# Kernel optimization log

Measured on AMD Instinct MI355X. Metric: run time of the kernel, lower is better.

Reference implementation:

```python
import jax, jax.numpy as jnp
import numpy as np

B, N, C, CODE, DIRB = 4, 321408, 3, 7, 2
K_PRE, K_POST = 1000, 300
IOU_THR, SCORE_THR, DIR_OFFSET = 0.5, 0.05, 0.0
POST_RANGE = np.array([0.0, -39.68, -5.0, 69.12, 39.68, 5.0], dtype=np.float32)


def setup_inputs() -> dict:
    key = jax.random.key(0)
    k1, k2, k3, k4 = jax.random.split(key, 4)
    box_preds = jax.random.normal(k1, (B, N, CODE), jnp.float32) * 0.3
    # shift logits down so sigmoid scores straddle the 0.05 threshold realistically
    cls_preds = jax.random.normal(k2, (B, N, C), jnp.float32) * 2.0 - 2.0
    dir_preds = jax.random.normal(k3, (B, N, DIRB), jnp.float32)
    ka, kb, kc = jax.random.split(k4, 3)
    xy = jax.random.uniform(ka, (N, 2), jnp.float32) * jnp.array([69.12, 79.36], jnp.float32) + jnp.array([0.0, -39.68], jnp.float32)
    z = jnp.full((N, 1), -1.0, jnp.float32)
    dims = jax.random.uniform(kb, (N, 3), jnp.float32, minval=1.0, maxval=4.0)
    rot = jax.random.randint(kc, (N, 1), 0, 2).astype(jnp.float32) * np.float32(np.pi / 2)
    anchors = jnp.concatenate([xy, z, dims, rot], axis=-1)
    return {"box_preds": box_preds, "cls_preds": cls_preds, "dir_preds": dir_preds, "anchors": anchors}


def _decode(deltas, anchors):
    # SECOND / PointPillars GroundBox3dCoder decode. anchors: [x,y,z,w,l,h,r]
    xa, ya, za, wa, la, ha, ra = (anchors[..., i] for i in range(7))
    xt, yt, zt, wt, lt, ht, rt = (deltas[..., i] for i in range(7))
    za = za + ha * 0.5
    diag = jnp.sqrt(la * la + wa * wa)
    xg = xt * diag + xa
    yg = yt * diag + ya
    zg = zt * ha + za
    wg = jnp.exp(wt) * wa
    lg = jnp.exp(lt) * la
    hg = jnp.exp(ht) * ha
    zg = zg - hg * 0.5
    rg = rt + ra
    return jnp.stack([xg, yg, zg, wg, lg, hg, rg], axis=-1)


def _nms_single(boxes7, scores, valid):
    # boxes_for_nms = box[:, [0,1,3,4,-1]] -> rotated (x,y,w,l,r); standup AABB of corners
    x, y, w, l, r = boxes7[:, 0], boxes7[:, 1], boxes7[:, 3], boxes7[:, 4], boxes7[:, 6]
    c, s = jnp.abs(jnp.cos(r)), jnp.abs(jnp.sin(r))
    hx = 0.5 * (w * c + l * s)   # half-extent of rotated corners along x
    hy = 0.5 * (w * s + l * c)
    x1, x2, y1, y2 = x - hx, x + hx, y - hy, y + hy
    area = (x2 - x1) * (y2 - y1)
    ix = jnp.clip(jnp.minimum(x2[:, None], x2[None, :]) - jnp.maximum(x1[:, None], x1[None, :]), 0.0)
    iy = jnp.clip(jnp.minimum(y2[:, None], y2[None, :]) - jnp.maximum(y1[:, None], y1[None, :]), 0.0)
    inter = ix * iy
    union = area[:, None] + area[None, :] - inter
    iou = jnp.where(union > 0, inter / jnp.maximum(union, 1e-12), 0.0)
    iou = jax.lax.stop_gradient(iou)
    idxs = jnp.arange(K_PRE)

    def body(keep, i):
        sup = keep[i] & (iou[i] > IOU_THR) & (idxs > i)
        return keep & ~sup, None

    keep, _ = jax.lax.scan(body, valid, idxs)
    rank = jnp.cumsum(keep) - 1                       # rank among kept (score order)
    pos = jnp.argsort(jnp.where(keep, rank, K_PRE))   # stable: kept-in-order first
    sel = pos[:K_POST]
    return sel, keep[sel]


def reference(box_preds, cls_preds, dir_preds, anchors):
    decoded = _decode(box_preds, anchors[None, :, :])          # [B,N,7]
    probs = jax.nn.sigmoid(cls_preds)                          # [B,N,C]
    top_scores = probs.max(axis=-1)
    top_labels = probs.argmax(axis=-1).astype(jnp.int32)
    dir_labels = dir_preds.argmax(axis=-1).astype(jnp.int32)
    valid = top_scores >= SCORE_THR
    sc_masked = jnp.where(valid, top_scores, -1.0)
    sc_k, idx = jax.lax.top_k(sc_masked, K_PRE)                # [B,K_PRE]
    boxes_k = jnp.take_along_axis(decoded, idx[..., None], axis=1)
    labels_k = jnp.take_along_axis(top_labels, idx, axis=1)
    dir_k = jnp.take_along_axis(dir_labels, idx, axis=1)
    valid_k = sc_k >= SCORE_THR
    sel, keep = jax.vmap(_nms_single)(boxes_k, sc_k, valid_k)  # [B,K_POST]
    boxes = jnp.take_along_axis(boxes_k, sel[..., None], axis=1)
    scores = jnp.take_along_axis(sc_k, sel, axis=1)
    labels = jnp.take_along_axis(labels_k, sel, axis=1)
    dirs = jnp.take_along_axis(dir_k, sel, axis=1)
    # direction flip: add pi where predicted direction disagrees with yaw sign
    opp = ((boxes[..., 6] - DIR_OFFSET) > 0) ^ (dirs == 1)
    r_fixed = boxes[..., 6] + jnp.where(opp, np.float32(np.pi), np.float32(0.0))
    boxes = jnp.concatenate([boxes[..., :6], r_fixed[..., None]], axis=-1)
    # post center-range filter
    lo = jnp.asarray(POST_RANGE[:3])
    hi = jnp.asarray(POST_RANGE[3:])
    in_range = jnp.all(boxes[..., :3] >= lo, axis=-1) & jnp.all(boxes[..., :3] <= hi, axis=-1)
    valid_out = keep & in_range
    boxes = jnp.where(valid_out[..., None], boxes, 0.0)
    scores = jnp.where(valid_out, scores, 0.0)
    labels = jnp.where(valid_out, labels, 0)
    return boxes, labels, scores, valid_out
```

## Files before the change

kernel.cpp:

```cpp
#include <hip/hip_runtime.h>
#include <stdint.h>

typedef unsigned long long u64;
typedef unsigned int u32;

#define BB 4
#define NN 321408
#define K_PRE 1000
#define K_POST 300
#define CAP 4096
#define NW 16
#define SCORE_THR 0.05f
#define IOU_THR 0.5f
#define SB 314
#define CH2 1024
#define NBINS 576
#define BIN0 0xBD4Cu
#define RED 8
#define RCH 40

__device__ __forceinline__ float sigm(float x) { return 1.0f / (1.0f + expf(-x)); }

__device__ __forceinline__ u32 mkkey(float mx) {
    float s = sigm(mx);
    return (s >= SCORE_THR) ? (__float_as_uint(s) | 0x80000000u) : 0u;
}

__global__ void k_score_hist(const float* __restrict__ cls, u32* __restrict__ key, u32* __restrict__ bh) {
    __shared__ u32 h1[NBINS], h2[NBINS];
    int bb = blockIdx.x, tid = threadIdx.x;
    int b = bb / SB, c = bb % SB;
    for (int i = tid; i < NBINS; i += 256) h1[i] = 0;
    __syncthreads();
    int a0 = c * CH2 + tid * 4;
    if (a0 < NN) {
        const float4* c4 = (const float4*)(cls + ((size_t)b * NN + a0) * 3);
        float4 v0 = c4[0], v1 = c4[1], v2 = c4[2];
        uint4 o;
        o.x = mkkey(fmaxf(v0.x, fmaxf(v0.y, v0.z)));
        o.y = mkkey(fmaxf(v0.w, fmaxf(v1.x, v1.y)));
        o.z = mkkey(fmaxf(v1.z, fmaxf(v1.w, v2.x)));
        o.w = mkkey(fmaxf(v2.y, fmaxf(v2.z, v2.w)));
        *((uint4*)(key + (size_t)b * NN + a0)) = o;
        if (o.x) atomicAdd(&h1[min((o.x >> 16) - BIN0, (u32)(NBINS - 1))], 1u);
        if (o.y) atomicAdd(&h1[min((o.y >> 16) - BIN0, (u32)(NBINS - 1))], 1u);
        if (o.z) atomicAdd(&h1[min((o.z >> 16) - BIN0, (u32)(NBINS - 1))], 1u);
        if (o.w) atomicAdd(&h1[min((o.w >> 16) - BIN0, (u32)(NBINS - 1))], 1u);
    }
    __syncthreads();
    u32* src = h1; u32* dst = h2;
    for (int off = 1; off < NBINS; off <<= 1) {
        for (int i = tid; i < NBINS; i += 256)
            dst[i] = src[i] + ((i + off < NBINS) ? src[i + off] : 0u);
        __syncthreads();
        u32* t = src; src = dst; dst = t;
    }
    for (int i = tid; i < NBINS; i += 256) bh[(size_t)bb * NBINS + i] = src[i];
}

__global__ __launch_bounds__(64) void k_red(const u32* __restrict__ bh, u32* __restrict__ part) {
    int blk = blockIdx.x, tid = threadIdx.x;
    int b = blk / (RED * 9);
    int r = (blk / 9) % RED;
    int g = blk % 9;
    int f = g * 64 + tid;
    int s0 = r * RCH, s1 = s0 + RCH; if (s1 > SB) s1 = SB;
    const u32* base = bh + (size_t)(b * SB + s0) * NBINS + f;
    u32 acc = 0;
    int n = s1 - s0;
    #pragma unroll 8
    for (int s = 0; s < n; ++s) acc += base[(size_t)s * NBINS];
    part[(size_t)(b * RED + r) * NBINS + f] = acc;
}

__global__ __launch_bounds__(256) void k_scatterT(const u32* __restrict__ key, const u32* __restrict__ part,
                                                  const u32* __restrict__ bh, u32* __restrict__ cnt,
                                                  u64* __restrict__ cand) {
    __shared__ u32 tot[NBINS];
    __shared__ u32 wtot[4];
    __shared__ u32 sTf;
    int bb = blockIdx.x, tid = threadIdx.x;
    int b = bb / SB, c = bb % SB;
    int lane = tid & 63, wv = tid >> 6;
    for (int f = tid; f < NBINS; f += 256) {
        u32 x = 0;
        #pragma unroll
        for (int r = 0; r < RED; ++r) x += part[(size_t)(b * RED + r) * NBINS + f];
        tot[f] = x;
    }
    __syncthreads();
    u32 tv = tot[0];
    u32 target = (tv < K_PRE) ? tv : K_PRE;
    if (target == 0) {
        if (c == 0 && tid == 0) cnt[b] = 0;
        return;
    }
    for (int f = tid; f < NBINS; f += 256) {
        u32 cge = tot[f];
        u32 cnx = (f + 1 < NBINS) ? tot[f + 1] : 0u;
        if (cge >= target && cnx < target) sTf = (u32)f;
    }
    __syncthreads();
    u32 Tf = sTf;
    if (c == 0 && tid == 0) cnt[b] = tot[Tf];
    u32 m = 0;
    if (tid < c) m = bh[(size_t)(b * SB + tid) * NBINS + Tf];
    if (tid + 256 < c) m += bh[(size_t)(b * SB + tid + 256) * NBINS + Tf];
    #pragma unroll
    for (int o = 32; o > 0; o >>= 1) m += __shfl_down(m, o);
    if (lane == 0) wtot[wv] = m;
    __syncthreads();
    u32 boffc = wtot[0] + wtot[1] + wtot[2] + wtot[3];
    __syncthreads();
    u32 T16 = BIN0 + Tf;
    int a0 = c * CH2 + tid * 4;
    uint4 kk = make_uint4(0u, 0u, 0u, 0u);
    if (a0 < NN) kk = *((const uint4*)(key + (size_t)b * NN + a0));
    u32 ks[4] = {kk.x, kk.y, kk.z, kk.w};
    u32 f4[4];
    #pragma unroll
    for (int e = 0; e < 4; ++e) f4[e] = (u32)((ks[e] != 0) && ((ks[e] >> 16) >= T16));
    u32 tc = f4[0] + f4[1] + f4[2] + f4[3];
    u32 x = tc;
    #pragma unroll
    for (int o = 1; o < 64; o <<= 1) {
        u32 y = __shfl_up(x, o);
        if (lane >= o) x += y;
    }
    if (lane == 63) wtot[wv] = x;
    __syncthreads();
    u32 base = 0;
    { u32 w0 = wtot[0], w1 = wtot[1], w2 = wtot[2];
      if (wv > 0) base += w0; if (wv > 1) base += w1; if (wv > 2) base += w2; }
    u32 pos = boffc + base + x - tc;
    u64* cb = cand + (size_t)b * CAP;
    #pragma unroll
    for (int e = 0; e < 4; ++e) {
        if (f4[e]) {
            if (pos < CAP) cb[pos] = ((u64)(~ks[e]) << 32) | (u64)(a0 + e);
            ++pos;
        }
    }
}

__global__ __launch_bounds__(256) void k_rankdec(const u32* __restrict__ cnt, const u64* __restrict__ cand,
                                                 const float* __restrict__ boxp, const float* __restrict__ cls,
                                                 const float* __restrict__ dirp, const float* __restrict__ anch,
                                                 float* __restrict__ tks, u32* __restrict__ meta,
                                                 float* __restrict__ box7, float* __restrict__ cor) {
    __shared__ u64 ck[CAP];
    int blk = blockIdx.x, tid = threadIdx.x;
    int b = blk >> 4, rb = blk & 15;
    u32 nc = cnt[b]; if (nc > CAP) nc = CAP;
    int ci = rb * 256 + tid;
    if (rb * 256 >= (int)nc && rb * 256 >= K_PRE) return;
    const u64* cb = cand + (size_t)b * CAP;
    for (int i = tid; i < (int)nc; i += 256) ck[i] = cb[i];
    __syncthreads();

    int rank = -1; u32 idx = 0xFFFFFFFFu;
    if (ci < (int)nc) {
        u64 my = ck[ci];
        u32 r = 0;
        int j = 0;
        int nlim = (int)nc & ~15;
        for (; j < nlim; j += 16) {
            u64 v0 = ck[j+0], v1 = ck[j+1], v2 = ck[j+2], v3 = ck[j+3];
            u64 v4 = ck[j+4], v5 = ck[j+5], v6 = ck[j+6], v7 = ck[j+7];
            u64 v8 = ck[j+8], v9 = ck[j+9], va = ck[j+10], vb = ck[j+11];
            u64 vc = ck[j+12], vd = ck[j+13], ve = ck[j+14], vf = ck[j+15];
            r += (u32)(v0 < my) + (u32)(v1 < my) + (u32)(v2 < my) + (u32)(v3 < my)
               + (u32)(v4 < my) + (u32)(v5 < my) + (u32)(v6 < my) + (u32)(v7 < my)
               + (u32)(v8 < my) + (u32)(v9 < my) + (u32)(va < my) + (u32)(vb < my)
               + (u32)(vc < my) + (u32)(vd < my) + (u32)(ve < my) + (u32)(vf < my);
        }
        for (; j < (int)nc; ++j) r += (u32)(ck[j] < my);
        if (r < K_PRE) { rank = (int)r; idx = (u32)my; }
    } else if (ci < K_PRE) {
        rank = ci;
    }
    if (rank < 0) return;

    float ob[7] = {0,0,0,0,0,0,0};
    float c5[5] = {0,0,0,0,0};
    float sc = 0.f; u32 mt = 0;
    if (idx != 0xFFFFFFFFu) {
        const float* A = anch + (size_t)idx * 7;
        const float* D = boxp + ((size_t)b * NN + idx) * 7;
        float xa=A[0], ya=A[1], za=A[2], wa=A[3], la=A[4], ha=A[5], ra=A[6];
        float xt=D[0], yt=D[1], zt=D[2], wt=D[3], lt=D[4], ht=D[5], rt=D[6];
        za = za + ha * 0.5f;
        float diag = sqrtf(la * la + wa * wa);
        float xg = xt * diag + xa;
        float yg = yt * diag + ya;
        float zg = zt * ha + za;
        float wg = expf(wt) * wa;
        float lg = expf(lt) * la;
        float hg = expf(ht) * ha;
        zg = zg - hg * 0.5f;
        float rg = rt + ra;
        ob[0]=xg; ob[1]=yg; ob[2]=zg; ob[3]=wg; ob[4]=lg; ob[5]=hg; ob[6]=rg;
        float cr = fabsf(cosf(rg)), sr = fabsf(sinf(rg));
        float hx = 0.5f * (wg * cr + lg * sr);
        float hy = 0.5f * (wg * sr + lg * cr);
        float x1 = xg - hx, x2 = xg + hx, y1 = yg - hy, y2 = yg + hy;
        c5[0]=x1; c5[1]=x2; c5[2]=y1; c5[3]=y2; c5[4]=(x2-x1)*(y2-y1);
        const float* cc = cls + ((size_t)b * NN + idx) * 3;
        float p0 = sigm(cc[0]), p1 = sigm(cc[1]), p2 = sigm(cc[2]);
        int lbl = 0; float best = p0;
        if (p1 > best) { best = p1; lbl = 1; }
        if (p2 > best) { best = p2; lbl = 2; }
        sc = best;
        const float* dd = dirp + ((size_t)b * NN + idx) * 2;
        int dl = (dd[1] > dd[0]) ? 1 : 0;
        mt = (u32)lbl | ((u32)dl << 8) | (1u << 16);
    }
    size_t t = (size_t)b * K_PRE + rank;
    tks[t] = sc; meta[t] = mt;
    #pragma unroll
    for (int j = 0; j < 7; ++j) box7[t * 7 + j] = ob[j];
    #pragma unroll
    for (int j = 0; j < 5; ++j) cor[t * 5 + j] = c5[j];
}

__global__ __launch_bounds__(256) void k_maskT(const float* __restrict__ cor, u64* __restrict__ maskT) {
    __shared__ float s4[(K_PRE + 16) * 4];
    __shared__ float sA[K_PRE + 16];
    int blk = blockIdx.x;
    int b = blk / 63, jb = blk % 63;
    int tid = threadIdx.x;
    const float4* C4 = (const float4*)(cor + (size_t)b * K_PRE * 5);
    for (int q = tid; q < (K_PRE * 5) / 4; q += 256) {
        float4 v = C4[q];
        int t0 = q * 4;
        #pragma unroll
        for (int e = 0; e < 4; ++e) {
            int t = t0 + e;
            int i = t / 5, k = t - i * 5;
            float val = (e == 0) ? v.x : (e == 1) ? v.y : (e == 2) ? v.z : v.w;
            int ip = i + (i >> 6);
            if (k < 4) s4[ip * 4 + k] = val; else sA[ip] = val;
        }
    }
    __syncthreads();
    int w = tid & 15, jl = tid >> 4;
    int j = jb * 16 + jl;
    if (j >= K_PRE) return;
    int jp = j + (j >> 6);
    float x1 = s4[jp*4+0], x2 = s4[jp*4+1], y1 = s4[jp*4+2], y2 = s4[jp*4+3], ar = sA[jp];
    u64 m = 0;
    int i0 = w * 64;
    if (i0 < j) {
        int iend = j - i0; if (iend > 64) iend = 64;
        for (int ii = 0; ii < iend; ++ii) {
            int i = i0 + ii;
            int ip = i + (i >> 6);
            float4 bx = *(const float4*)&s4[ip * 4];
            float ai = sA[ip];
            float ix = fminf(x2, bx.y) - fmaxf(x1, bx.x); ix = fmaxf(ix, 0.f);
            float iy = fminf(y2, bx.w) - fmaxf(y1, bx.z); iy = fmaxf(iy, 0.f);
            float inter = ix * iy;
            float uni = ai + ar - inter;
            float iou = (uni > 0.f) ? inter / fmaxf(uni, 1e-12f) : 0.f;
            if (iou > IOU_THR) m |= (1ull << ii);
        }
    }
    maskT[((size_t)b * K_PRE + j) * NW + w] = m;
}

__global__ __launch_bounds__(256) void k_nms_out(const u32* __restrict__ meta, const float* __restrict__ box7,
                                                 const float* __restrict__ tks, const u64* __restrict__ maskT,
                                                 float* __restrict__ out) {
    int b = blockIdx.x; int tid = threadIdx.x;
    __shared__ u64 km_s[16];
    __shared__ int sel_s[K_POST];
    __shared__ int cnt_s;
    if (tid < 16) km_s[tid] = 0ull;
    __syncthreads();
    if (tid < 64) {
        int lane = tid;
        const u32* M = meta + b * K_PRE;
        int cnt = 0; bool done = false;
        for (int c = 0; c < 16; ++c) {
            if (done) break;
            int j = c * 64 + lane;
            int jc = (j < K_PRE) ? j : (K_PRE - 1);
            bool jvalid = (j < K_PRE) && ((M[jc] >> 16) & 1u);
            const u64* colp = maskT + ((size_t)b * K_PRE + jc) * NW;
            u64 cw = 0; u64 supacc = 0;
            #pragma unroll
            for (int w = 0; w < 16; ++w) {
                u64 cv = colp[w];
                supacc |= (cv & km_s[w]);
                if (w == c) cw = cv;
            }
            u64 active = __ballot(jvalid && (supacc == 0ull));
            u64 kmc = 0;
            while (active) {
                int i = __ffsll((unsigned long long)active) - 1;
                if (lane == 0) sel_s[cnt] = c * 64 + i;
                ++cnt;
                if (cnt >= K_POST) { done = true; break; }
                kmc |= (1ull << i);
                u64 supb = __ballot(((cw >> i) & 1ull) != 0ull);
                active &= ~supb;
                active &= ~(1ull << i);
            }
            if (lane == 0) km_s[c] = kmc;
        }
        if (lane == 0) cnt_s = cnt;
    }
    __syncthreads();
    int cnt = cnt_s;
    const u32* M = meta + b * K_PRE;
    const float* BX = box7 + (size_t)b * K_PRE * 7;
    const float* SS = tks + b * K_PRE;
    for (int p = tid; p < K_POST; p += 256) {
        float ob[7] = {0,0,0,0,0,0,0};
        float sc = 0.f, lb = 0.f, vd = 0.f;
        if (p < cnt) {
            int i = sel_s[p];
            float xg = BX[i*7+0], yg = BX[i*7+1], zg = BX[i*7+2];
            bool in_range = (xg >= 0.0f) && (xg <= 69.12f) &&
                            (yg >= -39.68f) && (yg <= 39.68f) &&
                            (zg >= -5.0f) && (zg <= 5.0f);
            if (in_range) {
                u32 mt = M[i];
                int dl = (mt >> 8) & 0xFF;
                float r = BX[i*7+6];
                bool opp = ((r > 0.0f) != (dl == 1));
                float rf = r + (opp ? 3.14159274f : 0.0f);
                ob[0]=xg; ob[1]=yg; ob[2]=zg; ob[3]=BX[i*7+3]; ob[4]=BX[i*7+4]; ob[5]=BX[i*7+5]; ob[6]=rf;
                sc = SS[i]; lb = (float)(mt & 0xFF); vd = 1.0f;
            }
        }
        size_t ro = (size_t)(b * K_POST + p);
        #pragma unroll
        for (int j = 0; j < 7; ++j) out[ro * 7 + j] = ob[j];
        out[(size_t)BB * K_POST * 7 + ro] = lb;
        out[(size_t)BB * K_POST * 8 + ro] = sc;
        out[(size_t)BB * K_POST * 9 + ro] = vd;
    }
}

extern "C" void kernel_launch(void* const* d_in, const int* in_sizes, int n_in,
                              void* d_out, int out_size, void* d_ws, size_t ws_size,
                              hipStream_t stream) {
    const float* boxp = (const float*)d_in[0];
    const float* cls  = (const float*)d_in[1];
    const float* dirp = (const float*)d_in[2];
    const float* anch = (const float*)d_in[3];
    float* out = (float*)d_out;

    char* p = (char*)d_ws;
    u32* key  = (u32*)p; p += (size_t)BB * NN * 4;
    u32* bh   = (u32*)p; p += (size_t)BB * SB * NBINS * 4;
    u32* part = (u32*)p; p += (size_t)BB * RED * NBINS * 4;
    u32* cnt  = (u32*)p; p += 256;
    u64* cand = (u64*)p; p += (size_t)BB * CAP * 8;
    float* tks = (float*)p; p += (size_t)BB * K_PRE * 4;
    u32* meta = (u32*)p; p += (size_t)BB * K_PRE * 4;
    float* box7 = (float*)p; p += (size_t)BB * K_PRE * 7 * 4;
    float* cor  = (float*)p; p += (size_t)BB * K_PRE * 5 * 4;
    u64* maskT = (u64*)p; p += (size_t)BB * K_PRE * NW * 8;

    k_score_hist<<<BB * SB, 256, 0, stream>>>(cls, key, bh);
    k_red<<<BB * RED * 9, 64, 0, stream>>>(bh, part);
    k_scatterT<<<BB * SB, 256, 0, stream>>>(key, part, bh, cnt, cand);
    k_rankdec<<<BB * 16, 256, 0, stream>>>(cnt, cand, boxp, cls, dirp, anch, tks, meta, box7, cor);
    k_maskT<<<BB * 63, 256, 0, stream>>>(cor, maskT);
    k_nms_out<<<BB, 256, 0, stream>>>(meta, box7, tks, maskT, out);
}
```

Baseline: 87.15 us.

## Double-buffer NMS mask chunks in LDS with all 256 threads prefetching

```diff
diff --git a/kernel.cpp b/kernel.cpp
--- a/kernel.cpp
+++ b/kernel.cpp
@@ -272,28 +272,49 @@
                                                  const float* __restrict__ tks, const u64* __restrict__ maskT,
                                                  float* __restrict__ out) {
     int b = blockIdx.x; int tid = threadIdx.x;
+    int lane = tid & 63, wvi = tid >> 6;
+    __shared__ u64 mbuf[2][64][17];
+    __shared__ u64 vb_s[16];
     __shared__ u64 km_s[16];
     __shared__ int sel_s[K_POST];
     __shared__ int cnt_s;
+    const u32* M = meta + b * K_PRE;
+    const u64* Mk = maskT + (size_t)b * K_PRE * NW;
+
+    for (int base = 0; base < K_PRE; base += 256) {
+        int slot = base + tid;
+        bool v = (slot < K_PRE) && ((M[(slot < K_PRE) ? slot : 0] >> 16) & 1u);
+        u64 word = __ballot(v);
+        if (lane == 0) vb_s[(base >> 6) + wvi] = word;
+    }
     if (tid < 16) km_s[tid] = 0ull;
-    __syncthreads();
-    if (tid < 64) {
-        int lane = tid;
-        const u32* M = meta + b * K_PRE;
-        int cnt = 0; bool done = false;
-        for (int c = 0; c < 16; ++c) {
-            if (done) break;
+    {
+        int r = tid >> 2, w0 = (tid & 3) << 2;
+        const u64* s = Mk + (size_t)(0 * 64 + r) * NW + w0;
+        mbuf[0][r][w0+0] = s[0]; mbuf[0][r][w0+1] = s[1];
+        mbuf[0][r][w0+2] = s[2]; mbuf[0][r][w0+3] = s[3];
+    }
+    __syncthreads();
+
+    int cnt = 0; bool done = false;
+    for (int c = 0; c < 16; ++c) {
+        u64 a0 = 0, a1 = 0, a2 = 0, a3 = 0;
+        int r = tid >> 2, w0 = (tid & 3) << 2;
+        bool pf = (c + 1 < 16);
+        if (pf) {
+            int jn = (c + 1) * 64 + r;
+            int jcn = (jn < K_PRE) ? jn : (K_PRE - 1);
+            const u64* s = Mk + (size_t)jcn * NW + w0;
+            a0 = s[0]; a1 = s[1]; a2 = s[2]; a3 = s[3];
+        }
+        if (tid < 64 && !done) {
+            int p = c & 1;
+            u64 cw = mbuf[p][lane][c];
+            u64 supacc = 0;
+            #pragma unroll
+            for (int w = 0; w < 16; ++w) supacc |= (mbuf[p][lane][w] & km_s[w]);
             int j = c * 64 + lane;
-            int jc = (j < K_PRE) ? j : (K_PRE - 1);
-            bool jvalid = (j < K_PRE) && ((M[jc] >> 16) & 1u);
-            const u64* colp = maskT + ((size_t)b * K_PRE + jc) * NW;
-            u64 cw = 0; u64 supacc = 0;
-            #pragma unroll
-            for (int w = 0; w < 16; ++w) {
-                u64 cv = colp[w];
-                supacc |= (cv & km_s[w]);
-                if (w == c) cw = cv;
-            }
+            bool jvalid = (j < K_PRE) && (((vb_s[c] >> lane) & 1ull) != 0ull);
             u64 active = __ballot(jvalid && (supacc == 0ull));
             u64 kmc = 0;
             while (active) {
@@ -306,19 +327,25 @@
                 active &= ~supb;
                 active &= ~(1ull << i);
             }
-            if (lane == 0) km_s[c] = kmc;
-        }
-        if (lane == 0) cnt_s = cnt;
-    }
-    __syncthreads();
-    int cnt = cnt_s;
-    const u32* M = meta + b * K_PRE;
+            km_s[c] = kmc;
+        }
+        if (pf) {
+            int pn = (c + 1) & 1;
+            mbuf[pn][r][w0+0] = a0; mbuf[pn][r][w0+1] = a1;
+            mbuf[pn][r][w0+2] = a2; mbuf[pn][r][w0+3] = a3;
+        }
+        __syncthreads();
+    }
+    if (tid == 0) cnt_s = cnt;
+    __syncthreads();
+
+    int kept = cnt_s;
     const float* BX = box7 + (size_t)b * K_PRE * 7;
     const float* SS = tks + b * K_PRE;
     for (int p = tid; p < K_POST; p += 256) {
         float ob[7] = {0,0,0,0,0,0,0};
         float sc = 0.f, lb = 0.f, vd = 0.f;
-        if (p < cnt) {
+        if (p < kept) {
             int i = sel_s[p];
             float xg = BX[i*7+0], yg = BX[i*7+1], zg = BX[i*7+2];
             bool in_range = (xg >= 0.0f) && (xg <= 69.12f) &&
```

After: 106.5 us. 22.3% more time.
